# Kernel tuning notes

Measured on AMD Instinct MI355X. Metric: run time of the kernel, lower is better.

The kernel has to match this reference:

```python
import jax, jax.numpy as jnp
import numpy as np

B, L, NUM_AA, E, H = 128, 2048, 20, 16, 128

def _mlp(x, W1, b1, W2, b2, W3, b3):
    h = jax.nn.relu(x @ W1 + b1)
    h = jax.nn.relu(h @ W2 + b2)
    return h @ W3 + b3

def _mlp_params(key, in_dim):
    k1, k2, k3 = jax.random.split(key, 3)
    W1 = jax.random.normal(k1, (in_dim, H), jnp.float32) / np.sqrt(in_dim)
    W2 = jax.random.normal(k2, (H, H), jnp.float32) / np.sqrt(H)
    W3 = jax.random.normal(k3, (H, 1), jnp.float32) / np.sqrt(H)
    return W1, jnp.zeros((H,), jnp.float32), W2, jnp.zeros((H,), jnp.float32), W3, jnp.zeros((1,), jnp.float32)

def setup_inputs() -> dict:
    key = jax.random.key(0)
    kR, ks, ke, kl, kt, kp = jax.random.split(key, 6)
    inp = {
        'R': jax.random.normal(kR, (B, L, 3), jnp.float32) * 3.8,  # ~CA-CA scale
        'seq': jax.random.randint(ks, (B, L), 0, NUM_AA),
        'emb': jax.random.normal(ke, (NUM_AA, E), jnp.float32),
    }
    for pref, k, d in (('fl', kl, 1 + 2 * E), ('ft', kt, 1 + 3 * E), ('fp', kp, 2 + 4 * E)):
        W1, b1, W2, b2, W3, b3 = _mlp_params(k, d)
        inp.update({f'{pref}_W1': W1, f'{pref}_b1': b1, f'{pref}_W2': W2, f'{pref}_b2': b2, f'{pref}_W3': W3, f'{pref}_b3': b3})
    return inp

def _energy(R, e, fl, ft, fp):
    d = R[:, 1:, :] - R[:, :-1, :]                      # [B,L-1,3] bond vectors
    lengths = jnp.linalg.norm(d, axis=-1)               # [B,L-1]
    x_l = jnp.concatenate([lengths[..., None], e[:, :-1, :], e[:, 1:, :]], axis=-1)
    E_l = _mlp(x_l, *fl)[..., 0].sum(axis=1)
    # bond angles at atom i+1 between (R[i]-R[i+1]) and (R[i+2]-R[i+1])
    u, v = -d[:, :-1, :], d[:, 1:, :]                   # [B,L-2,3]
    cos_t = jnp.sum(u * v, axis=-1) / (jnp.linalg.norm(u, axis=-1) * jnp.linalg.norm(v, axis=-1))
    theta_in = jnp.clip(cos_t, -1.0, 1.0)               # use_cos_theta=True -> cos(arccos(clip))
    x_t = jnp.concatenate([theta_in[..., None], e[:, :-2, :], e[:, 1:-1, :], e[:, 2:, :]], axis=-1)
    E_t = _mlp(x_t, *ft)[..., 0].sum(axis=1)
    # torsions over quadruples
    b1, b2, b3 = d[:, :-2, :], d[:, 1:-1, :], d[:, 2:, :]
    n1 = jnp.cross(b1, b2)
    n2 = jnp.cross(b2, b3)
    b2u = b2 / jnp.linalg.norm(b2, axis=-1, keepdims=True)
    m1 = jnp.cross(n1, b2u)
    phi = jnp.arctan2(jnp.sum(m1 * n2, axis=-1), jnp.sum(n1 * n2, axis=-1))  # [B,L-3]
    sc = jnp.stack([jnp.sin(phi), jnp.cos(phi)], axis=-1)                    # [B,L-3,2]
    x_p = jnp.concatenate([sc, e[:, :-3, :], e[:, 1:-2, :], e[:, 2:-1, :], e[:, 3:, :]], axis=-1)
    E_p = _mlp(x_p, *fp)[..., 0].sum(axis=1)
    return E_l + E_t + E_p

def reference(R, seq, emb,
              fl_W1, fl_b1, fl_W2, fl_b2, fl_W3, fl_b3,
              ft_W1, ft_b1, ft_W2, ft_b2, ft_W3, ft_b3,
              fp_W1, fp_b1, fp_W2, fp_b2, fp_W3, fp_b3):
    e = emb[seq]                                        # [B,L,E]
    return _energy(R, e,
                   (fl_W1, fl_b1, fl_W2, fl_b2, fl_W3, fl_b3),
                   (ft_W1, ft_b1, ft_W2, ft_b2, ft_W3, ft_b3),
                   (fp_W1, fp_b1, fp_W2, fp_b2, fp_W3, fp_b3))
```

## Files before the change

kernel.cpp:

```cpp
#include <hip/hip_runtime.h>


typedef short bf16x8  __attribute__((ext_vector_type(8)));
typedef float f32x4   __attribute__((ext_vector_type(4)));
typedef float f32x16  __attribute__((ext_vector_type(16)));

constexpr int Lc  = 2048;

union FragU { uint4 u; bf16x8 v; };

__device__ __forceinline__ unsigned short f2bf(float f) {
    union { float f; unsigned u; } v; v.f = f;
    unsigned u = v.u;
    u = u + 0x7FFFu + ((u >> 16) & 1u);
    return (unsigned short)(u >> 16);
}

__device__ __forceinline__ unsigned pkbf(float a, float b) {
    unsigned ua = __float_as_uint(a) + 0x8000u;
    unsigned ub = __float_as_uint(b) + 0x8000u;
    return __builtin_amdgcn_perm(ub, ua, 0x07060302u);
}

__global__ __launch_bounds__(256)
void prep_kernel(const float* __restrict__ W1_0, const float* __restrict__ b1_0,
                 const float* __restrict__ W1_1, const float* __restrict__ b1_1,
                 const float* __restrict__ W1_2, const float* __restrict__ b1_2,
                 const float* __restrict__ W2_0, const float* __restrict__ W2_1,
                 const float* __restrict__ W2_2,
                 const float* __restrict__ emb, char* __restrict__ ws,
                 float* __restrict__ out)
{
    const int tid = blockIdx.x * 256 + threadIdx.x;
    const int np  = gridDim.x * 256;
    if (blockIdx.x == 0 && threadIdx.x < 128) out[threadIdx.x] = 0.0f;

    unsigned short* d2 = (unsigned short*)ws;
    for (int o = tid; o < 3 * 16384; o += np) {
        int t = o >> 14, r = o & 16383, col = r >> 7, k = r & 127;
        const float* W2 = (t == 0) ? W2_0 : (t == 1) ? W2_1 : W2_2;
        d2[o] = f2bf(W2[k * 128 + col]);
    }
    unsigned short* d1 = (unsigned short*)(ws + 98304);
    for (int o = tid; o < 3 * 12288; o += np) {
        int t = o / 12288, r = o - t * 12288, hid = r / 96, k = r - hid * 96;
        const int NE16 = (t == 0) ? 32 : (t == 1) ? 48 : 64;
        const int NG   = (t == 2) ? 2 : 1;
        const float* W1 = (t == 0) ? W1_0 : (t == 1) ? W1_1 : W1_2;
        const float* b1 = (t == 0) ? b1_0 : (t == 1) ? b1_1 : b1_2;
        float v = 0.0f;
        if (k >= 16) {
            int j = k - 16;
            if (j < NE16) v = W1[(NG + j) * 128 + hid];
        } else if (k == 4) v = b1[hid];
        else if (t == 0 && k == 0) v = W1_0[hid];
        else if (t == 1 && k == 1) v = W1_1[hid];
        else if (t == 2 && k == 2) v = W1_2[hid];
        else if (t == 2 && k == 3) v = W1_2[128 + hid];
        d1[o] = f2bf(v);
    }
    unsigned short* eb = (unsigned short*)(ws + 172032);
    for (int i = tid; i < 320; i += np) eb[i] = f2bf(emb[i]);
}

struct SMem {
    unsigned short H1s[128 * 128];
    float  Rbuf[393];
    uint2  geomh[128];
    int    seqb[132];
    alignas(16) unsigned short ebuf[320];
    float  part[4];
};

__device__ __forceinline__ int h1_off(int row, int col2x ) {
    return row * 256 + (col2x ^ ((row & 15) << 4));
}

template<int TYPE>
__device__ __forceinline__ void type_pass(
    SMem& sm, const char* __restrict__ ws,
    const float* __restrict__ b2, const float* __restrict__ w3,
    int i0, int wv, int ln31, int hi, f32x4& p4)
{
    constexpr int NEMB  = (TYPE == 0) ? 2 : (TYPE == 1) ? 3 : 4;
    constexpr int STEPS = 1 + NEMB;
    constexpr int ROWSB = Lc - 1 - TYPE;

    const unsigned short* w1t = (const unsigned short*)(ws + 98304 + TYPE * 24576);
    const unsigned short* w2t = (const unsigned short*)(ws + TYPE * 32768);
    const f32x4 z4 = (f32x4){0.f, 0.f, 0.f, 0.f};

    FragU A1[STEPS];
#pragma unroll
    for (int s = 0; s < STEPS; ++s)
        A1[s].u = *(const uint4*)&w1t[(wv * 32 + ln31) * 96 + s * 16 + hi * 8];

#pragma unroll
    for (int h = 0; h < 2; ++h) {
        f32x16 acc1[2];
        acc1[0] = (f32x16)(0.f);
        acc1[1] = (f32x16)(0.f);

#pragma unroll
        for (int s = 0; s < STEPS; ++s) {
#pragma unroll
            for (int rt = 0; rt < 2; ++rt) {
                const int row = h * 64 + rt * 32 + ln31;
                FragU bb;
                if (s == 0) {
                    if (hi == 0) {
                        uint2 g = sm.geomh[row];
                        bb.u = make_uint4(g.x, g.y, 0x00003F80u, 0u);
                    } else {
                        bb.u = make_uint4(0u, 0u, 0u, 0u);
                    }
                } else {
                    bb.u = *(const uint4*)&sm.ebuf[sm.seqb[row + (s - 1)] * 16 + hi * 8];
                }
                acc1[rt] = __builtin_amdgcn_mfma_f32_32x32x16_bf16(A1[s].v, bb.v, acc1[rt], 0, 0, 0);
            }
        }

#pragma unroll
        for (int rt = 0; rt < 2; ++rt) {
            const int row = h * 64 + rt * 32 + ln31;
#pragma unroll
            for (int g = 0; g < 4; ++g) {
                float v0 = fmaxf(acc1[rt][4 * g + 0], 0.f);
                float v1 = fmaxf(acc1[rt][4 * g + 1], 0.f);
                float v2 = fmaxf(acc1[rt][4 * g + 2], 0.f);
                float v3 = fmaxf(acc1[rt][4 * g + 3], 0.f);
                uint2 pk;
                pk.x = pkbf(v0, v1);
                pk.y = pkbf(v2, v3);
                *(uint2*)((char*)sm.H1s + h1_off(row, wv * 64 + 16 * g + 8 * hi)) = pk;
            }
        }
    }

    FragU B2[8];
#pragma unroll
    for (int s2 = 0; s2 < 8; ++s2)
        B2[s2].u = *(const uint4*)&w2t[(wv * 32 + ln31) * 128 + s2 * 16 + hi * 8];
    const float b2v = b2[wv * 32 + ln31];
    const float w3v = w3[wv * 32 + ln31];
    __syncthreads();

#pragma unroll
    for (int h = 0; h < 2; ++h) {
        f32x16 acc2[2];
        acc2[0] = (f32x16)(0.f);
        acc2[1] = (f32x16)(0.f);
#pragma unroll
        for (int s2 = 0; s2 < 8; ++s2)
#pragma unroll
            for (int rt = 0; rt < 2; ++rt) {
                const int row = h * 64 + rt * 32 + ln31;
                bf16x8 aa = *(const bf16x8*)((const char*)sm.H1s +
                                             h1_off(row, s2 * 32 + hi * 16));
                acc2[rt] = __builtin_amdgcn_mfma_f32_32x32x16_bf16(aa, B2[s2].v, acc2[rt], 0, 0, 0);
            }

#pragma unroll
        for (int rt = 0; rt < 2; ++rt) {
#pragma unroll
            for (int g = 0; g < 4; ++g) {
                const int rbase = i0 + h * 64 + rt * 32 + 8 * g + 4 * hi;
                f32x4 v;
                v[0] = acc2[rt][4 * g + 0]; v[1] = acc2[rt][4 * g + 1];
                v[2] = acc2[rt][4 * g + 2]; v[3] = acc2[rt][4 * g + 3];
                v = __builtin_elementwise_max(v + b2v, z4);
                if (rbase + 3 < ROWSB) {
                    p4 += v * w3v;
                } else {
#pragma unroll
                    for (int rg = 0; rg < 4; ++rg)
                        if (rbase + rg < ROWSB) p4[rg] += v[rg] * w3v;
                }
            }
        }
    }
    __syncthreads();
}

__global__ __launch_bounds__(256, 4)
void energy_kernel(const float* __restrict__ R, const int* __restrict__ seq,
                   const char* __restrict__ ws,
                   const float* b2_0, const float* b2_1, const float* b2_2,
                   const float* w3_0, const float* w3_1, const float* w3_2,
                   const float* b3_0, const float* b3_1, const float* b3_2,
                   float* __restrict__ out)
{
    __shared__ SMem sm;
    const int tid = threadIdx.x;
    const int b   = blockIdx.y;
    const int i0  = blockIdx.x * 128;
    const int lane = tid & 63, wv = tid >> 6;
    const int ln31 = lane & 31, hi = lane >> 5;

    for (int t = tid; t < 393; t += 256) {
        int lr = t / 3, comp = t - lr * 3;
        int row = min(i0 + lr, Lc - 1);
        sm.Rbuf[t] = R[((size_t)b * Lc + row) * 3 + comp];
    }
    for (int t = tid; t < 131; t += 256)
        sm.seqb[t] = seq[b * Lc + min(i0 + t, Lc - 1)];
    {
        const uint4* se = (const uint4*)(ws + 172032);
        for (int t = tid; t < 40; t += 256) ((uint4*)sm.ebuf)[t] = se[t];
    }
    __syncthreads();

    if (tid < 128) {
        const float* p0 = &sm.Rbuf[tid * 3];
        float ax = p0[3] - p0[0], ay = p0[4] - p0[1], az = p0[5] - p0[2];
        float bx = p0[6] - p0[3], by = p0[7] - p0[4], bz = p0[8] - p0[5];
        float cx = p0[9] - p0[6], cy = p0[10] - p0[7], cz = p0[11] - p0[8];
        float na2 = ax * ax + ay * ay + az * az;
        float len = sqrtf(na2);
        float nb2 = bx * bx + by * by + bz * bz;
        float duv = -(ax * bx + ay * by + az * bz);
        float cost = fminf(fmaxf(duv / sqrtf(na2 * nb2), -1.0f), 1.0f);
        float n1x = ay * bz - az * by, n1y = az * bx - ax * bz, n1z = ax * by - ay * bx;
        float n2x = by * cz - bz * cy, n2y = bz * cx - bx * cz, n2z = bx * cy - by * cx;
        float binv = 1.0f / sqrtf(nb2);
        float ux = bx * binv, uy = by * binv, uz = bz * binv;
        float m1x = n1y * uz - n1z * uy, m1y = n1z * ux - n1x * uz, m1z = n1x * uy - n1y * ux;
        float yv = m1x * n2x + m1y * n2y + m1z * n2z;
        float xv = n1x * n2x + n1y * n2y + n1z * n2z;
        float inv = 1.0f / sqrtf(xv * xv + yv * yv);
        sm.geomh[tid] = make_uint2(pkbf(len, cost), pkbf(yv * inv, xv * inv));
    }
    __syncthreads();

    f32x4 p4 = (f32x4){0.f, 0.f, 0.f, 0.f};
    type_pass<0>(sm, ws, b2_0, w3_0, i0, wv, ln31, hi, p4);
    type_pass<1>(sm, ws, b2_1, w3_1, i0, wv, ln31, hi, p4);
    type_pass<2>(sm, ws, b2_2, w3_2, i0, wv, ln31, hi, p4);

    float p = p4[0] + p4[1] + p4[2] + p4[3];
#pragma unroll
    for (int off = 32; off > 0; off >>= 1)
        p += __shfl_down(p, off);
    if (lane == 0) sm.part[wv] = p;
    __syncthreads();
    if (tid == 0) {
        float tot = sm.part[0] + sm.part[1] + sm.part[2] + sm.part[3];
        tot += b3_0[0] * (float)min(Lc - 1 - i0, 128);
        tot += b3_1[0] * (float)min(Lc - 2 - i0, 128);
        tot += b3_2[0] * (float)min(Lc - 3 - i0, 128);
        atomicAdd(&out[b], tot);
    }
}

extern "C" void kernel_launch(void* const* d_in, const int* in_sizes, int n_in,
                              void* d_out, int out_size, void* d_ws, size_t ws_size,
                              hipStream_t stream) {
    const float* R   = (const float*)d_in[0];
    const int*   seq = (const int*)d_in[1];
    const float* emb = (const float*)d_in[2];
    float* out = (float*)d_out;
    char*  ws  = (char*)d_ws;

    prep_kernel<<<dim3(96), dim3(256), 0, stream>>>(
        (const float*)d_in[3],  (const float*)d_in[4],
        (const float*)d_in[9],  (const float*)d_in[10],
        (const float*)d_in[15], (const float*)d_in[16],
        (const float*)d_in[5],  (const float*)d_in[11], (const float*)d_in[17],
        emb, ws, out);

    dim3 grid(16, 128), block(256);
    energy_kernel<<<grid, block, 0, stream>>>(
        R, seq, ws,
        (const float*)d_in[6],  (const float*)d_in[12], (const float*)d_in[18],
        (const float*)d_in[7],  (const float*)d_in[13], (const float*)d_in[19],
        (const float*)d_in[8],  (const float*)d_in[14], (const float*)d_in[20],
        out);
}
```

Baseline: 146.8 us.

## Halve H1 shared buffer, interleave layer passes per half, use hardware bf16 pack

The two MLP layers now run per 64-row half instead of all 128 rows, so the layer-1 activation buffer in shared memory shrinks by half and more blocks can fit per CU. Layer-2 weights are loaded before layer 1 so the loads overlap with it, and the bias is folded into the accumulator's initial value. bf16 packing switches from a manual add-and-permute to the v_cvt_pk_bf16_f32 instruction, and the embedding table is padded to stride 24 to cut LDS bank conflicts. The cost is more block-wide barriers per pass and higher register pressure from holding the layer-2 weights earlier.

```diff
diff --git a/kernel.cpp b/kernel.cpp
--- a/kernel.cpp
+++ b/kernel.cpp
@@ -16,10 +16,10 @@
     return (unsigned short)(u >> 16);
 }
 
-__device__ __forceinline__ unsigned pkbf(float a, float b) {
-    unsigned ua = __float_as_uint(a) + 0x8000u;
-    unsigned ub = __float_as_uint(b) + 0x8000u;
-    return __builtin_amdgcn_perm(ub, ua, 0x07060302u);
+__device__ __forceinline__ unsigned cvtpk(float a, float b) {
+    unsigned r;
+    asm("v_cvt_pk_bf16_f32 %0, %1, %2" : "=v"(r) : "v"(a), "v"(b));
+    return r;
 }
 
 __global__ __launch_bounds__(256)
@@ -64,16 +64,16 @@
 }
 
 struct SMem {
-    unsigned short H1s[128 * 128];
+    unsigned short H1s[64 * 128];
     float  Rbuf[393];
     uint2  geomh[128];
     int    seqb[132];
-    alignas(16) unsigned short ebuf[320];
+    alignas(16) unsigned short ebuf[20 * 24];
     float  part[4];
 };
 
-__device__ __forceinline__ int h1_off(int row, int col2x ) {
-    return row * 256 + (col2x ^ ((row & 15) << 4));
+__device__ __forceinline__ int h1_off(int lr, int colb) {
+    return lr * 256 + (colb ^ ((lr & 15) << 4));
 }
 
 template<int TYPE>
@@ -94,13 +94,18 @@
 #pragma unroll
     for (int s = 0; s < STEPS; ++s)
         A1[s].u = *(const uint4*)&w1t[(wv * 32 + ln31) * 96 + s * 16 + hi * 8];
+    FragU B2[8];
+#pragma unroll
+    for (int s2 = 0; s2 < 8; ++s2)
+        B2[s2].u = *(const uint4*)&w2t[(wv * 32 + ln31) * 128 + s2 * 16 + hi * 8];
+    const float b2v = b2[wv * 32 + ln31];
+    const float w3v = w3[wv * 32 + ln31];
 
 #pragma unroll
     for (int h = 0; h < 2; ++h) {
         f32x16 acc1[2];
         acc1[0] = (f32x16)(0.f);
         acc1[1] = (f32x16)(0.f);
-
 #pragma unroll
         for (int s = 0; s < STEPS; ++s) {
 #pragma unroll
@@ -115,7 +120,7 @@
                         bb.u = make_uint4(0u, 0u, 0u, 0u);
                     }
                 } else {
-                    bb.u = *(const uint4*)&sm.ebuf[sm.seqb[row + (s - 1)] * 16 + hi * 8];
+                    bb.u = *(const uint4*)&sm.ebuf[sm.seqb[row + (s - 1)] * 24 + hi * 8];
                 }
                 acc1[rt] = __builtin_amdgcn_mfma_f32_32x32x16_bf16(A1[s].v, bb.v, acc1[rt], 0, 0, 0);
             }
@@ -123,7 +128,7 @@
 
 #pragma unroll
         for (int rt = 0; rt < 2; ++rt) {
-            const int row = h * 64 + rt * 32 + ln31;
+            const int lr = rt * 32 + ln31;
 #pragma unroll
             for (int g = 0; g < 4; ++g) {
                 float v0 = fmaxf(acc1[rt][4 * g + 0], 0.f);
@@ -131,33 +136,23 @@
                 float v2 = fmaxf(acc1[rt][4 * g + 2], 0.f);
                 float v3 = fmaxf(acc1[rt][4 * g + 3], 0.f);
                 uint2 pk;
-                pk.x = pkbf(v0, v1);
-                pk.y = pkbf(v2, v3);
-                *(uint2*)((char*)sm.H1s + h1_off(row, wv * 64 + 16 * g + 8 * hi)) = pk;
-            }
-        }
-    }
-
-    FragU B2[8];
-#pragma unroll
-    for (int s2 = 0; s2 < 8; ++s2)
-        B2[s2].u = *(const uint4*)&w2t[(wv * 32 + ln31) * 128 + s2 * 16 + hi * 8];
-    const float b2v = b2[wv * 32 + ln31];
-    const float w3v = w3[wv * 32 + ln31];
-    __syncthreads();
-
-#pragma unroll
-    for (int h = 0; h < 2; ++h) {
+                pk.x = cvtpk(v0, v1);
+                pk.y = cvtpk(v2, v3);
+                *(uint2*)((char*)sm.H1s + h1_off(lr, wv * 64 + 16 * g + 8 * hi)) = pk;
+            }
+        }
+        __syncthreads();
+
         f32x16 acc2[2];
-        acc2[0] = (f32x16)(0.f);
-        acc2[1] = (f32x16)(0.f);
+        acc2[0] = (f32x16)(b2v);
+        acc2[1] = (f32x16)(b2v);
 #pragma unroll
         for (int s2 = 0; s2 < 8; ++s2)
 #pragma unroll
             for (int rt = 0; rt < 2; ++rt) {
-                const int row = h * 64 + rt * 32 + ln31;
+                const int lr = rt * 32 + ln31;
                 bf16x8 aa = *(const bf16x8*)((const char*)sm.H1s +
-                                             h1_off(row, s2 * 32 + hi * 16));
+                                             h1_off(lr, s2 * 32 + hi * 16));
                 acc2[rt] = __builtin_amdgcn_mfma_f32_32x32x16_bf16(aa, B2[s2].v, acc2[rt], 0, 0, 0);
             }
 
@@ -169,7 +164,7 @@
                 f32x4 v;
                 v[0] = acc2[rt][4 * g + 0]; v[1] = acc2[rt][4 * g + 1];
                 v[2] = acc2[rt][4 * g + 2]; v[3] = acc2[rt][4 * g + 3];
-                v = __builtin_elementwise_max(v + b2v, z4);
+                v = __builtin_elementwise_max(v, z4);
                 if (rbase + 3 < ROWSB) {
                     p4 += v * w3v;
                 } else {
@@ -179,8 +174,8 @@
                 }
             }
         }
-    }
-    __syncthreads();
+        __syncthreads();
+    }
 }
 
 __global__ __launch_bounds__(256, 4)
@@ -207,7 +202,10 @@
         sm.seqb[t] = seq[b * Lc + min(i0 + t, Lc - 1)];
     {
         const uint4* se = (const uint4*)(ws + 172032);
-        for (int t = tid; t < 40; t += 256) ((uint4*)sm.ebuf)[t] = se[t];
+        for (int t = tid; t < 40; t += 256) {
+            int aa = t >> 1, half = t & 1;
+            *(uint4*)&sm.ebuf[aa * 24 + half * 8] = se[t];
+        }
     }
     __syncthreads();
 
@@ -229,7 +227,7 @@
         float yv = m1x * n2x + m1y * n2y + m1z * n2z;
         float xv = n1x * n2x + n1y * n2y + n1z * n2z;
         float inv = 1.0f / sqrtf(xv * xv + yv * yv);
-        sm.geomh[tid] = make_uint2(pkbf(len, cost), pkbf(yv * inv, xv * inv));
+        sm.geomh[tid] = make_uint2(cvtpk(len, cost), cvtpk(yv * inv, xv * inv));
     }
     __syncthreads();
 
```

Result: slower. 155.4 us (+5.9%).

## Repartition second MLP layer by rows per wave, stream W2 column tiles

Applied to the files above, without the earlier changes.

The second-layer GEMM is re-split so each wave owns 32 rows of H1 and loops over all four 32-column tiles of W2. Previously each wave held one W2 column slice and read all 128 H1 rows from LDS. Now the wave's H1 A-fragments are loaded from LDS once and reused across column tiles, while W2 fragments are fetched from global memory or cache per tile. This cuts LDS traffic but adds global weight loads, and a single accumulator chain per tile reduces independent MFMA streams.

```diff
diff --git a/kernel.cpp b/kernel.cpp
--- a/kernel.cpp
+++ b/kernel.cpp
@@ -72,8 +72,8 @@
     float  part[4];
 };
 
-__device__ __forceinline__ int h1_off(int row, int col2x ) {
-    return row * 256 + (col2x ^ ((row & 15) << 4));
+__device__ __forceinline__ int h1_off(int row, int colb) {
+    return row * 256 + (colb ^ ((row & 15) << 4));
 }
 
 template<int TYPE>
@@ -138,45 +138,41 @@
         }
     }
 
-    FragU B2[8];
+    __syncthreads();
+
+    FragU a2f[8];
 #pragma unroll
     for (int s2 = 0; s2 < 8; ++s2)
-        B2[s2].u = *(const uint4*)&w2t[(wv * 32 + ln31) * 128 + s2 * 16 + hi * 8];
-    const float b2v = b2[wv * 32 + ln31];
-    const float w3v = w3[wv * 32 + ln31];
-    __syncthreads();
-
-#pragma unroll
-    for (int h = 0; h < 2; ++h) {
-        f32x16 acc2[2];
-        acc2[0] = (f32x16)(0.f);
-        acc2[1] = (f32x16)(0.f);
+        a2f[s2].u = *(const uint4*)((const char*)sm.H1s +
+                                    h1_off(wv * 32 + ln31, s2 * 32 + hi * 16));
+
+#pragma unroll
+    for (int ct = 0; ct < 4; ++ct) {
+        FragU B2[8];
 #pragma unroll
         for (int s2 = 0; s2 < 8; ++s2)
-#pragma unroll
-            for (int rt = 0; rt < 2; ++rt) {
-                const int row = h * 64 + rt * 32 + ln31;
-                bf16x8 aa = *(const bf16x8*)((const char*)sm.H1s +
-                                             h1_off(row, s2 * 32 + hi * 16));
-                acc2[rt] = __builtin_amdgcn_mfma_f32_32x32x16_bf16(aa, B2[s2].v, acc2[rt], 0, 0, 0);
-            }
-
-#pragma unroll
-        for (int rt = 0; rt < 2; ++rt) {
-#pragma unroll
-            for (int g = 0; g < 4; ++g) {
-                const int rbase = i0 + h * 64 + rt * 32 + 8 * g + 4 * hi;
-                f32x4 v;
-                v[0] = acc2[rt][4 * g + 0]; v[1] = acc2[rt][4 * g + 1];
-                v[2] = acc2[rt][4 * g + 2]; v[3] = acc2[rt][4 * g + 3];
-                v = __builtin_elementwise_max(v + b2v, z4);
-                if (rbase + 3 < ROWSB) {
-                    p4 += v * w3v;
-                } else {
-#pragma unroll
-                    for (int rg = 0; rg < 4; ++rg)
-                        if (rbase + rg < ROWSB) p4[rg] += v[rg] * w3v;
-                }
+            B2[s2].u = *(const uint4*)&w2t[(ct * 32 + ln31) * 128 + s2 * 16 + hi * 8];
+        const float b2v = b2[ct * 32 + ln31];
+        const float w3v = w3[ct * 32 + ln31];
+
+        f32x16 acc2 = (f32x16)(0.f);
+#pragma unroll
+        for (int s2 = 0; s2 < 8; ++s2)
+            acc2 = __builtin_amdgcn_mfma_f32_32x32x16_bf16(a2f[s2].v, B2[s2].v, acc2, 0, 0, 0);
+
+#pragma unroll
+        for (int g = 0; g < 4; ++g) {
+            const int rbase = i0 + wv * 32 + 8 * g + 4 * hi;
+            f32x4 v;
+            v[0] = acc2[4 * g + 0]; v[1] = acc2[4 * g + 1];
+            v[2] = acc2[4 * g + 2]; v[3] = acc2[4 * g + 3];
+            v = __builtin_elementwise_max(v + b2v, z4);
+            if (rbase + 3 < ROWSB) {
+                p4 += v * w3v;
+            } else {
+#pragma unroll
+                for (int rg = 0; rg < 4; ++rg)
+                    if (rbase + rg < ROWSB) p4[rg] += v[rg] * w3v;
             }
         }
     }
```

After: 198.6 us. 35.3% more time.

## Split row halves across 8 waves per block instead of looping in 4

Applied to the files above, without the earlier changes.

The block grows from 256 to 512 threads. Each of 8 waves now handles one 32-hidden-unit slice (hq) for one 64-row half (hh), replacing the loop over two halves inside each of 4 waves. This doubles the waves available to hide MFMA and LDS latency within a block and shortens each wave's serial chain. In exchange, each weight fragment is loaded by two waves, the launch bound of 512 threads with 4 blocks may limit registers per thread, and shared-memory use per block stays the same while the thread count doubles.

```diff
diff --git a/kernel.cpp b/kernel.cpp
--- a/kernel.cpp
+++ b/kernel.cpp
@@ -69,18 +69,18 @@
     uint2  geomh[128];
     int    seqb[132];
     alignas(16) unsigned short ebuf[320];
-    float  part[4];
+    float  part[8];
 };
 
-__device__ __forceinline__ int h1_off(int row, int col2x ) {
-    return row * 256 + (col2x ^ ((row & 15) << 4));
+__device__ __forceinline__ int h1_off(int row, int colb) {
+    return row * 256 + (colb ^ ((row & 15) << 4));
 }
 
 template<int TYPE>
 __device__ __forceinline__ void type_pass(
     SMem& sm, const char* __restrict__ ws,
     const float* __restrict__ b2, const float* __restrict__ w3,
-    int i0, int wv, int ln31, int hi, f32x4& p4)
+    int i0, int hq, int hh, int ln31, int hi, f32x4& p4)
 {
     constexpr int NEMB  = (TYPE == 0) ? 2 : (TYPE == 1) ? 3 : 4;
     constexpr int STEPS = 1 + NEMB;
@@ -93,97 +93,91 @@
     FragU A1[STEPS];
 #pragma unroll
     for (int s = 0; s < STEPS; ++s)
-        A1[s].u = *(const uint4*)&w1t[(wv * 32 + ln31) * 96 + s * 16 + hi * 8];
-
-#pragma unroll
-    for (int h = 0; h < 2; ++h) {
-        f32x16 acc1[2];
-        acc1[0] = (f32x16)(0.f);
-        acc1[1] = (f32x16)(0.f);
-
-#pragma unroll
-        for (int s = 0; s < STEPS; ++s) {
-#pragma unroll
-            for (int rt = 0; rt < 2; ++rt) {
-                const int row = h * 64 + rt * 32 + ln31;
-                FragU bb;
-                if (s == 0) {
-                    if (hi == 0) {
-                        uint2 g = sm.geomh[row];
-                        bb.u = make_uint4(g.x, g.y, 0x00003F80u, 0u);
-                    } else {
-                        bb.u = make_uint4(0u, 0u, 0u, 0u);
-                    }
+        A1[s].u = *(const uint4*)&w1t[(hq * 32 + ln31) * 96 + s * 16 + hi * 8];
+
+    f32x16 acc1[2];
+    acc1[0] = (f32x16)(0.f);
+    acc1[1] = (f32x16)(0.f);
+
+#pragma unroll
+    for (int s = 0; s < STEPS; ++s) {
+#pragma unroll
+        for (int rt = 0; rt < 2; ++rt) {
+            const int row = hh * 64 + rt * 32 + ln31;
+            FragU bb;
+            if (s == 0) {
+                if (hi == 0) {
+                    uint2 g = sm.geomh[row];
+                    bb.u = make_uint4(g.x, g.y, 0x00003F80u, 0u);
                 } else {
-                    bb.u = *(const uint4*)&sm.ebuf[sm.seqb[row + (s - 1)] * 16 + hi * 8];
+                    bb.u = make_uint4(0u, 0u, 0u, 0u);
                 }
-                acc1[rt] = __builtin_amdgcn_mfma_f32_32x32x16_bf16(A1[s].v, bb.v, acc1[rt], 0, 0, 0);
+            } else {
+                bb.u = *(const uint4*)&sm.ebuf[sm.seqb[row + (s - 1)] * 16 + hi * 8];
             }
-        }
-
+            acc1[rt] = __builtin_amdgcn_mfma_f32_32x32x16_bf16(A1[s].v, bb.v, acc1[rt], 0, 0, 0);
+        }
+    }
+
+#pragma unroll
+    for (int rt = 0; rt < 2; ++rt) {
+        const int row = hh * 64 + rt * 32 + ln31;
+#pragma unroll
+        for (int g = 0; g < 4; ++g) {
+            float v0 = fmaxf(acc1[rt][4 * g + 0], 0.f);
+            float v1 = fmaxf(acc1[rt][4 * g + 1], 0.f);
+            float v2 = fmaxf(acc1[rt][4 * g + 2], 0.f);
+            float v3 = fmaxf(acc1[rt][4 * g + 3], 0.f);
+            uint2 pk;
+            pk.x = pkbf(v0, v1);
+            pk.y = pkbf(v2, v3);
+            *(uint2*)((char*)sm.H1s + h1_off(row, hq * 64 + 16 * g + 8 * hi)) = pk;
+        }
+    }
+
+    FragU B2[8];
+#pragma unroll
+    for (int s2 = 0; s2 < 8; ++s2)
+        B2[s2].u = *(const uint4*)&w2t[(hq * 32 + ln31) * 128 + s2 * 16 + hi * 8];
+    const float b2v = b2[hq * 32 + ln31];
+    const float w3v = w3[hq * 32 + ln31];
+    __syncthreads();
+
+    f32x16 acc2[2];
+    acc2[0] = (f32x16)(0.f);
+    acc2[1] = (f32x16)(0.f);
+#pragma unroll
+    for (int s2 = 0; s2 < 8; ++s2)
 #pragma unroll
         for (int rt = 0; rt < 2; ++rt) {
-            const int row = h * 64 + rt * 32 + ln31;
-#pragma unroll
-            for (int g = 0; g < 4; ++g) {
-                float v0 = fmaxf(acc1[rt][4 * g + 0], 0.f);
-                float v1 = fmaxf(acc1[rt][4 * g + 1], 0.f);
-                float v2 = fmaxf(acc1[rt][4 * g + 2], 0.f);
-                float v3 = fmaxf(acc1[rt][4 * g + 3], 0.f);
-                uint2 pk;
-                pk.x = pkbf(v0, v1);
-                pk.y = pkbf(v2, v3);
-                *(uint2*)((char*)sm.H1s + h1_off(row, wv * 64 + 16 * g + 8 * hi)) = pk;
+            const int row = hh * 64 + rt * 32 + ln31;
+            bf16x8 aa = *(const bf16x8*)((const char*)sm.H1s +
+                                         h1_off(row, s2 * 32 + hi * 16));
+            acc2[rt] = __builtin_amdgcn_mfma_f32_32x32x16_bf16(aa, B2[s2].v, acc2[rt], 0, 0, 0);
+        }
+
+#pragma unroll
+    for (int rt = 0; rt < 2; ++rt) {
+#pragma unroll
+        for (int g = 0; g < 4; ++g) {
+            const int rbase = i0 + hh * 64 + rt * 32 + 8 * g + 4 * hi;
+            f32x4 v;
+            v[0] = acc2[rt][4 * g + 0]; v[1] = acc2[rt][4 * g + 1];
+            v[2] = acc2[rt][4 * g + 2]; v[3] = acc2[rt][4 * g + 3];
+            v = __builtin_elementwise_max(v + b2v, z4);
+            if (rbase + 3 < ROWSB) {
+                p4 += v * w3v;
+            } else {
+#pragma unroll
+                for (int rg = 0; rg < 4; ++rg)
+                    if (rbase + rg < ROWSB) p4[rg] += v[rg] * w3v;
             }
         }
     }
-
-    FragU B2[8];
-#pragma unroll
-    for (int s2 = 0; s2 < 8; ++s2)
-        B2[s2].u = *(const uint4*)&w2t[(wv * 32 + ln31) * 128 + s2 * 16 + hi * 8];
-    const float b2v = b2[wv * 32 + ln31];
-    const float w3v = w3[wv * 32 + ln31];
-    __syncthreads();
-
-#pragma unroll
-    for (int h = 0; h < 2; ++h) {
-        f32x16 acc2[2];
-        acc2[0] = (f32x16)(0.f);
-        acc2[1] = (f32x16)(0.f);
-#pragma unroll
-        for (int s2 = 0; s2 < 8; ++s2)
-#pragma unroll
-            for (int rt = 0; rt < 2; ++rt) {
-                const int row = h * 64 + rt * 32 + ln31;
-                bf16x8 aa = *(const bf16x8*)((const char*)sm.H1s +
-                                             h1_off(row, s2 * 32 + hi * 16));
-                acc2[rt] = __builtin_amdgcn_mfma_f32_32x32x16_bf16(aa, B2[s2].v, acc2[rt], 0, 0, 0);
-            }
-
-#pragma unroll
-        for (int rt = 0; rt < 2; ++rt) {
-#pragma unroll
-            for (int g = 0; g < 4; ++g) {
-                const int rbase = i0 + h * 64 + rt * 32 + 8 * g + 4 * hi;
-                f32x4 v;
-                v[0] = acc2[rt][4 * g + 0]; v[1] = acc2[rt][4 * g + 1];
-                v[2] = acc2[rt][4 * g + 2]; v[3] = acc2[rt][4 * g + 3];
-                v = __builtin_elementwise_max(v + b2v, z4);
-                if (rbase + 3 < ROWSB) {
-                    p4 += v * w3v;
-                } else {
-#pragma unroll
-                    for (int rg = 0; rg < 4; ++rg)
-                        if (rbase + rg < ROWSB) p4[rg] += v[rg] * w3v;
-                }
-            }
-        }
-    }
-    __syncthreads();
-}
-
-__global__ __launch_bounds__(256, 4)
+    __syncthreads();
+}
+
+__global__ __launch_bounds__(512, 4)
 void energy_kernel(const float* __restrict__ R, const int* __restrict__ seq,
                    const char* __restrict__ ws,
                    const float* b2_0, const float* b2_1, const float* b2_2,
@@ -195,19 +189,20 @@
     const int tid = threadIdx.x;
     const int b   = blockIdx.y;
     const int i0  = blockIdx.x * 128;
-    const int lane = tid & 63, wv = tid >> 6;
+    const int lane = tid & 63, wv8 = tid >> 6;
     const int ln31 = lane & 31, hi = lane >> 5;
-
-    for (int t = tid; t < 393; t += 256) {
+    const int hq = wv8 & 3, hh = wv8 >> 2;
+
+    for (int t = tid; t < 393; t += 512) {
         int lr = t / 3, comp = t - lr * 3;
         int row = min(i0 + lr, Lc - 1);
         sm.Rbuf[t] = R[((size_t)b * Lc + row) * 3 + comp];
     }
-    for (int t = tid; t < 131; t += 256)
+    for (int t = tid; t < 131; t += 512)
         sm.seqb[t] = seq[b * Lc + min(i0 + t, Lc - 1)];
     {
         const uint4* se = (const uint4*)(ws + 172032);
-        for (int t = tid; t < 40; t += 256) ((uint4*)sm.ebuf)[t] = se[t];
+        for (int t = tid; t < 40; t += 512) ((uint4*)sm.ebuf)[t] = se[t];
     }
     __syncthreads();
 
@@ -234,18 +229,20 @@
     __syncthreads();
 
     f32x4 p4 = (f32x4){0.f, 0.f, 0.f, 0.f};
-    type_pass<0>(sm, ws, b2_0, w3_0, i0, wv, ln31, hi, p4);
-    type_pass<1>(sm, ws, b2_1, w3_1, i0, wv, ln31, hi, p4);
-    type_pass<2>(sm, ws, b2_2, w3_2, i0, wv, ln31, hi, p4);
+    type_pass<0>(sm, ws, b2_0, w3_0, i0, hq, hh, ln31, hi, p4);
+    type_pass<1>(sm, ws, b2_1, w3_1, i0, hq, hh, ln31, hi, p4);
+    type_pass<2>(sm, ws, b2_2, w3_2, i0, hq, hh, ln31, hi, p4);
 
     float p = p4[0] + p4[1] + p4[2] + p4[3];
 #pragma unroll
     for (int off = 32; off > 0; off >>= 1)
         p += __shfl_down(p, off);
-    if (lane == 0) sm.part[wv] = p;
+    if (lane == 0) sm.part[wv8] = p;
     __syncthreads();
     if (tid == 0) {
-        float tot = sm.part[0] + sm.part[1] + sm.part[2] + sm.part[3];
+        float tot = 0.f;
+#pragma unroll
+        for (int w = 0; w < 8; ++w) tot += sm.part[w];
         tot += b3_0[0] * (float)min(Lc - 1 - i0, 128);
         tot += b3_1[0] * (float)min(Lc - 2 - i0, 128);
         tot += b3_2[0] * (float)min(Lc - 3 - i0, 128);
@@ -269,7 +266,7 @@
         (const float*)d_in[5],  (const float*)d_in[11], (const float*)d_in[17],
         emb, ws, out);
 
-    dim3 grid(16, 128), block(256);
+    dim3 grid(16, 128), block(512);
     energy_kernel<<<grid, block, 0, stream>>>(
         R, seq, ws,
         (const float*)d_in[6],  (const float*)d_in[12], (const float*)d_in[18],
```

After: 169.1 us. +15.2%, slower.
